# Performance work log

Measured on AMD Instinct MI355X. Metric: run time of the kernel, lower is better.

## Reference

```python
import jax, jax.numpy as jnp
from jax import lax
import numpy as np
import math

D = 256; H = 4; DH = 64; PERIOD = 30; WIN = 4; L = 2
AUDIO = 768; MOTION = 33
B = 8; T = 1024; S = 1024


def _pe_table(t, d=D, period=PERIOD):
    pos = np.arange(period, dtype=np.float32)[:, None]
    div = np.exp(np.arange(0, d, 2, dtype=np.float32) * (-math.log(10000.0) / d))
    pe = np.zeros((period, d), np.float32)
    pe[:, 0::2] = np.sin(pos * div)
    pe[:, 1::2] = np.cos(pos * div)
    reps = t // period + 1
    return jnp.asarray(np.tile(pe, (reps, 1))[:t])


def _tgt_mask(t):
    # ALiBi-style bias (quantized by period) + causal mask, per head. [H,t,t]
    slopes = jnp.array([0.25 ** (i + 1) for i in range(H)], jnp.float32)
    i = jnp.arange(t)[:, None]
    j = jnp.arange(t)[None, :]
    rel = i - j
    alibi = jnp.where(rel >= 0, -(rel // PERIOD).astype(jnp.float32), 0.0)
    causal = jnp.where(rel >= 0, 0.0, -jnp.inf)
    return slopes[:, None, None] * alibi + causal[None]


def _mem_mask(t, s):
    i = jnp.arange(t)[:, None]
    j = jnp.arange(s)[None, :]
    return jnp.where(jnp.abs(i - j) <= WIN, 0.0, -jnp.inf)


def _ln(x, g, b, eps=1e-5):
    mu = jnp.mean(x, -1, keepdims=True)
    var = jnp.mean(jnp.square(x - mu), -1, keepdims=True)
    return (x - mu) * lax.rsqrt(var + eps) * g + b


def _mha(xq, xkv, in_w, in_b, out_w, out_b, mask):
    wq, wk, wv = jnp.split(in_w, 3, axis=0)
    bq, bk, bv = jnp.split(in_b, 3)
    q = xq @ wq.T + bq
    k = xkv @ wk.T + bk
    v = xkv @ wv.T + bv
    b_, t_, _ = q.shape
    s_ = k.shape[1]
    q = q.reshape(b_, t_, H, DH)
    k = k.reshape(b_, s_, H, DH)
    v = v.reshape(b_, s_, H, DH)
    scores = jnp.einsum('bthd,bshd->bhts', q, k) / math.sqrt(DH) + mask
    a = jax.nn.softmax(scores, axis=-1)
    o = jnp.einsum('bhts,bshd->bthd', a, v).reshape(b_, t_, D)
    return o @ out_w.T + out_b


def _conv1d(x_nch, w, b):
    y = lax.conv_general_dilated(x_nch, w, (1,), [(2, 2)],
                                 dimension_numbers=('NCH', 'OIH', 'NCH'))
    return y + b[None, :, None]


def setup_inputs() -> dict:
    key = jax.random.key(0)
    ks = iter(jax.random.split(key, 40))

    def r(shape, s=0.05):
        return jax.random.normal(next(ks), shape, jnp.float32) * s

    return {
        'hidden_states': jax.random.normal(next(ks), (B, S, AUDIO), jnp.float32),
        'target_motions': jax.random.uniform(next(ks), (B, T, MOTION), jnp.float32),
        'W_af': r((D, AUDIO)), 'b_af': r((D,)),
        'conv1_w': r((D, D, 5)), 'conv1_b': r((D,)),
        'conv2_w': r((D, D, 5)), 'conv2_b': r((D,)),
        'W_vm': r((D, MOTION)), 'b_vm': r((D,)),
        'sa_in_w': r((L, 3 * D, D)), 'sa_in_b': r((L, 3 * D)),
        'sa_out_w': r((L, D, D)), 'sa_out_b': r((L, D)),
        'ca_in_w': r((L, 3 * D, D)), 'ca_in_b': r((L, 3 * D)),
        'ca_out_w': r((L, D, D)), 'ca_out_b': r((L, D)),
        'ln1_g': jnp.ones((L, D)), 'ln1_b': jnp.zeros((L, D)),
        'ln2_g': jnp.ones((L, D)), 'ln2_b': jnp.zeros((L, D)),
        'ln3_g': jnp.ones((L, D)), 'ln3_b': jnp.zeros((L, D)),
        'ff1_w': r((L, 2 * D, D)), 'ff1_b': r((L, 2 * D)),
        'ff2_w': r((L, D, 2 * D)), 'ff2_b': r((L, D)),
        'W_vr': r((MOTION, D)), 'b_vr': r((MOTION,)),
    }


def reference(hidden_states, target_motions, W_af, b_af, conv1_w, conv1_b,
              conv2_w, conv2_b, W_vm, b_vm, sa_in_w, sa_in_b, sa_out_w,
              sa_out_b, ca_in_w, ca_in_b, ca_out_w, ca_out_b, ln1_g, ln1_b,
              ln2_g, ln2_b, ln3_g, ln3_b, ff1_w, ff1_b, ff2_w, ff2_b,
              W_vr, b_vr):
    # audio encoder: linear + residual temporal convs (exact GELU)
    audio = hidden_states @ W_af.T + b_af                       # [B,S,D]
    c = _conv1d(audio.transpose(0, 2, 1), conv1_w, conv1_b)
    c = jax.nn.gelu(c, approximate=False)
    c = _conv1d(c, conv2_w, conv2_b)
    audio = audio + c.transpose(0, 2, 1)

    b_, t_, _ = target_motions.shape
    motion_in = jnp.concatenate(
        [jnp.zeros((b_, 1, MOTION), target_motions.dtype),
         target_motions[:, :-1]], axis=1)
    x = motion_in @ W_vm.T + b_vm + _pe_table(t_)               # PPE (eval: no dropout)

    tm = _tgt_mask(t_)                                          # [H,t,t]
    mm = _mem_mask(t_, audio.shape[1])                          # [t,s]

    for l in range(L):  # post-norm TransformerDecoderLayer, relu FFN
        x = _ln(x + _mha(x, x, sa_in_w[l], sa_in_b[l], sa_out_w[l], sa_out_b[l], tm),
                ln1_g[l], ln1_b[l])
        x = _ln(x + _mha(x, audio, ca_in_w[l], ca_in_b[l], ca_out_w[l], ca_out_b[l], mm),
                ln2_g[l], ln2_b[l])
        h = jax.nn.relu(x @ ff1_w[l].T + ff1_b[l]) @ ff2_w[l].T + ff2_b[l]
        x = _ln(x + h, ln3_g[l], ln3_b[l])

    return jnp.clip(x @ W_vr.T + b_vr, 0.0, 1.0)
```

## Files before the change

### kernel.cpp

```cpp
#include <hip/hip_runtime.h>
#include <math.h>

#define B_ 8
#define T_ 1024
#define S_ 1024
#define D_ 256
#define H_ 4
#define DH_ 64
#define AUDIO_ 768
#define MOTION_ 33
#define PERIOD_ 30
#define WIN_ 4
#define M_ (B_ * T_)

typedef _Float16 half8 __attribute__((ext_vector_type(8)));
typedef _Float16 half4 __attribute__((ext_vector_type(4)));
typedef __attribute__((ext_vector_type(4))) float f32x4;

#define O_AF    0
#define O_SAIN  196608
#define O_SAOUT 589824
#define O_CAIN  720896
#define O_CAOUT 1114112
#define O_FF1   1245184
#define O_FF2   1507328
#define O_CONV1 1769472
#define O_CONV2 2097152
#define O_VR    2424832
#define WH_TOT  2441216
#define HID_TOT 6291456

struct CvtSrc { const float* p[17]; };

__global__ __launch_bounds__(256) void cvt_all(
    CvtSrc s, _Float16* __restrict__ wH, _Float16* __restrict__ hidH) {
  const long i = (long)blockIdx.x * 256 + threadIdx.x;
  if (i >= (long)WH_TOT + HID_TOT) return;
  if (i >= WH_TOT) { const long j = i - WH_TOT; hidH[j] = (_Float16)s.p[15][j]; return; }
  if (i >= O_VR) {
    const long j = i - O_VR, oc = j >> 8, cin = j & 255;
    wH[i] = (oc < MOTION_) ? (_Float16)s.p[16][oc * 256 + cin] : (_Float16)0.f;
    return;
  }
  if (i >= O_CONV2) {
    const long j = i - O_CONV2, oc = j / 1280, r = j % 1280, tap = r >> 8, cin = r & 255;
    wH[i] = (_Float16)s.p[14][(oc * 256 + cin) * 5 + tap]; return;
  }
  if (i >= O_CONV1) {
    const long j = i - O_CONV1, oc = j / 1280, r = j % 1280, tap = r >> 8, cin = r & 255;
    wH[i] = (_Float16)s.p[13][(oc * 256 + cin) * 5 + tap]; return;
  }
  int seg; long base;
  if      (i >= 1638400) { seg = 12; base = 1638400; }
  else if (i >= 1507328) { seg = 11; base = 1507328; }
  else if (i >= 1376256) { seg = 10; base = 1376256; }
  else if (i >= 1245184) { seg = 9;  base = 1245184; }
  else if (i >= 1179648) { seg = 8;  base = 1179648; }
  else if (i >= 1114112) { seg = 7;  base = 1114112; }
  else if (i >= 917504)  { seg = 6;  base = 917504; }
  else if (i >= 720896)  { seg = 5;  base = 720896; }
  else if (i >= 655360)  { seg = 4;  base = 655360; }
  else if (i >= 589824)  { seg = 3;  base = 589824; }
  else if (i >= 393216)  { seg = 2;  base = 393216; }
  else if (i >= 196608)  { seg = 1;  base = 196608; }
  else                   { seg = 0;  base = 0; }
  wH[i] = (_Float16)s.p[seg][i - base];
}

__global__ __launch_bounds__(256) void gemm_h(
    const _Float16* __restrict__ A, const _Float16* __restrict__ W,
    const float* __restrict__ bias, float* __restrict__ Cf,
    _Float16* __restrict__ Ch, int M, int N, int K, int relu) {
  __shared__ _Float16 As[2][64][72];
  __shared__ _Float16 Bs[2][64][72];
  const int tid = threadIdx.x;
  const int wave = tid >> 6, lane = tid & 63;
  const int wr = wave >> 1, wc = wave & 1;
  const int lr16 = lane & 15, kq = lane >> 4;
  const int bm = blockIdx.x, bn = blockIdx.y;
  const int sr = tid >> 2, sq = tid & 3;

  const _Float16* Ap = A + (size_t)(bm * 64 + sr) * K + sq * 8;
  const _Float16* Wp = W + (size_t)(bn * 64 + sr) * K + sq * 8;

  half8 ra0 = *reinterpret_cast<const half8*>(Ap);
  half8 ra1 = *reinterpret_cast<const half8*>(Ap + 32);
  half8 rw0 = *reinterpret_cast<const half8*>(Wp);
  half8 rw1 = *reinterpret_cast<const half8*>(Wp + 32);
  f32x4 acc[2][2] = {};

  *reinterpret_cast<half8*>(&As[0][sr][sq * 8]) = ra0;
  *reinterpret_cast<half8*>(&As[0][sr][32 + sq * 8]) = ra1;
  *reinterpret_cast<half8*>(&Bs[0][sr][sq * 8]) = rw0;
  *reinterpret_cast<half8*>(&Bs[0][sr][32 + sq * 8]) = rw1;
  __syncthreads();

  const int nsteps = K >> 6;
  for (int step = 0; step < nsteps; ++step) {
    const int cur = step & 1;
    const bool more = (step + 1 < nsteps);
    if (more) {
      const int kn = (step + 1) << 6;
      ra0 = *reinterpret_cast<const half8*>(Ap + kn);
      ra1 = *reinterpret_cast<const half8*>(Ap + kn + 32);
      rw0 = *reinterpret_cast<const half8*>(Wp + kn);
      rw1 = *reinterpret_cast<const half8*>(Wp + kn + 32);
    }
    half8 af[2][2], bf[2][2];
#pragma unroll
    for (int m = 0; m < 2; ++m)
#pragma unroll
      for (int s = 0; s < 2; ++s)
        af[m][s] = *reinterpret_cast<const half8*>(
            &As[cur][wr * 32 + m * 16 + lr16][s * 32 + kq * 8]);
#pragma unroll
    for (int n = 0; n < 2; ++n)
#pragma unroll
      for (int s = 0; s < 2; ++s)
        bf[n][s] = *reinterpret_cast<const half8*>(
            &Bs[cur][wc * 32 + n * 16 + lr16][s * 32 + kq * 8]);
#pragma unroll
    for (int m = 0; m < 2; ++m)
#pragma unroll
      for (int n = 0; n < 2; ++n)
#pragma unroll
        for (int s = 0; s < 2; ++s)
          acc[m][n] = __builtin_amdgcn_mfma_f32_16x16x32_f16(af[m][s], bf[n][s], acc[m][n], 0, 0, 0);
    if (more) {
      *reinterpret_cast<half8*>(&As[cur ^ 1][sr][sq * 8]) = ra0;
      *reinterpret_cast<half8*>(&As[cur ^ 1][sr][32 + sq * 8]) = ra1;
      *reinterpret_cast<half8*>(&Bs[cur ^ 1][sr][sq * 8]) = rw0;
      *reinterpret_cast<half8*>(&Bs[cur ^ 1][sr][32 + sq * 8]) = rw1;
      __syncthreads();
    }
  }

#pragma unroll
  for (int m = 0; m < 2; ++m) {
#pragma unroll
    for (int n = 0; n < 2; ++n) {
      const int col = bn * 64 + wc * 32 + n * 16 + lr16;
      const float bv = bias[col];
#pragma unroll
      for (int j = 0; j < 4; ++j) {
        const int row = bm * 64 + wr * 32 + m * 16 + kq * 4 + j;
        float v = acc[m][n][j] + bv;
        if (relu) v = fmaxf(v, 0.f);
        const size_t idx = (size_t)row * N + col;
        if (Cf) Cf[idx] = v;
        if (Ch) Ch[idx] = (_Float16)v;
      }
    }
  }
}

__global__ __launch_bounds__(256) void gemm_ca(
    const _Float16* __restrict__ Aq, const _Float16* __restrict__ Akv,
    const _Float16* __restrict__ W, const float* __restrict__ bias,
    _Float16* __restrict__ Oq, _Float16* __restrict__ Okv) {
  __shared__ _Float16 As[2][64][72];
  __shared__ _Float16 Bs[2][64][72];
  const int tid = threadIdx.x;
  const int wave = tid >> 6, lane = tid & 63;
  const int wr = wave >> 1, wc = wave & 1;
  const int lr16 = lane & 15, kq = lane >> 4;
  const int bm = blockIdx.x, bn = blockIdx.y;
  const int sr = tid >> 2, sq = tid & 3;
  const bool isq = (bn < 4);
  const _Float16* A = isq ? Aq : Akv;
  _Float16* Optr = isq ? Oq : Okv;
  const int Nout = isq ? 256 : 512;
  const int ocol0 = (isq ? bn : bn - 4) * 64;

  const _Float16* Ap = A + (size_t)(bm * 64 + sr) * 256 + sq * 8;
  const _Float16* Wp = W + (size_t)(bn * 64 + sr) * 256 + sq * 8;

  half8 ra0 = *reinterpret_cast<const half8*>(Ap);
  half8 ra1 = *reinterpret_cast<const half8*>(Ap + 32);
  half8 rw0 = *reinterpret_cast<const half8*>(Wp);
  half8 rw1 = *reinterpret_cast<const half8*>(Wp + 32);
  f32x4 acc[2][2] = {};

  *reinterpret_cast<half8*>(&As[0][sr][sq * 8]) = ra0;
  *reinterpret_cast<half8*>(&As[0][sr][32 + sq * 8]) = ra1;
  *reinterpret_cast<half8*>(&Bs[0][sr][sq * 8]) = rw0;
  *reinterpret_cast<half8*>(&Bs[0][sr][32 + sq * 8]) = rw1;
  __syncthreads();

  for (int step = 0; step < 4; ++step) {
    const int cur = step & 1;
    const bool more = (step + 1 < 4);
    if (more) {
      const int kn = (step + 1) << 6;
      ra0 = *reinterpret_cast<const half8*>(Ap + kn);
      ra1 = *reinterpret_cast<const half8*>(Ap + kn + 32);
      rw0 = *reinterpret_cast<const half8*>(Wp + kn);
      rw1 = *reinterpret_cast<const half8*>(Wp + kn + 32);
    }
    half8 af[2][2], bf[2][2];
#pragma unroll
    for (int m = 0; m < 2; ++m)
#pragma unroll
      for (int s = 0; s < 2; ++s)
        af[m][s] = *reinterpret_cast<const half8*>(
            &As[cur][wr * 32 + m * 16 + lr16][s * 32 + kq * 8]);
#pragma unroll
    for (int n = 0; n < 2; ++n)
#pragma unroll
      for (int s = 0; s < 2; ++s)
        bf[n][s] = *reinterpret_cast<const half8*>(
            &Bs[cur][wc * 32 + n * 16 + lr16][s * 32 + kq * 8]);
#pragma unroll
    for (int m = 0; m < 2; ++m)
#pragma unroll
      for (int n = 0; n < 2; ++n)
#pragma unroll
        for (int s = 0; s < 2; ++s)
          acc[m][n] = __builtin_amdgcn_mfma_f32_16x16x32_f16(af[m][s], bf[n][s], acc[m][n], 0, 0, 0);
    if (more) {
      *reinterpret_cast<half8*>(&As[cur ^ 1][sr][sq * 8]) = ra0;
      *reinterpret_cast<half8*>(&As[cur ^ 1][sr][32 + sq * 8]) = ra1;
      *reinterpret_cast<half8*>(&Bs[cur ^ 1][sr][sq * 8]) = rw0;
      *reinterpret_cast<half8*>(&Bs[cur ^ 1][sr][32 + sq * 8]) = rw1;
      __syncthreads();
    }
  }

#pragma unroll
  for (int m = 0; m < 2; ++m) {
#pragma unroll
    for (int n = 0; n < 2; ++n) {
      const int lc = wc * 32 + n * 16 + lr16;
      const float bv = bias[bn * 64 + lc];
#pragma unroll
      for (int j = 0; j < 4; ++j) {
        const int row = bm * 64 + wr * 32 + m * 16 + kq * 4 + j;
        Optr[(size_t)row * Nout + ocol0 + lc] = (_Float16)(acc[m][n][j] + bv);
      }
    }
  }
}

__device__ __forceinline__ half8 conv_ld(const _Float16* Xb, int p, int tap, int cin) {
  const int sp = p + tap - 2;
  if (sp < 0 || sp >= S_) { half8 z = {}; return z; }
  return *reinterpret_cast<const half8*>(Xb + (size_t)sp * D_ + cin);
}

__global__ __launch_bounds__(256) void conv_h(
    const _Float16* __restrict__ Xh, const _Float16* __restrict__ Wc,
    const float* __restrict__ bias, _Float16* OutH,
    const _Float16* ResH, int mode) {
  __shared__ _Float16 As[2][64][72];
  __shared__ _Float16 Bs[2][64][72];
  const int tid = threadIdx.x;
  const int wave = tid >> 6, lane = tid & 63;
  const int wr = wave >> 1, wc = wave & 1;
  const int lr16 = lane & 15, kq = lane >> 4;
  const int b = blockIdx.x >> 4;
  const int s0 = (blockIdx.x & 15) * 64;
  const int o0 = blockIdx.y * 64;
  const int sr = tid >> 2, sq = tid & 3;

  const _Float16* Xb = Xh + (size_t)b * S_ * D_;
  const _Float16* Wp = Wc + (size_t)(o0 + sr) * 1280 + sq * 8;
  const int p = s0 + sr;

  half8 ra0 = conv_ld(Xb, p, 0, sq * 8);
  half8 ra1 = conv_ld(Xb, p, 0, 32 + sq * 8);
  half8 rw0 = *reinterpret_cast<const half8*>(Wp);
  half8 rw1 = *reinterpret_cast<const half8*>(Wp + 32);
  f32x4 acc[2][2] = {};

  *reinterpret_cast<half8*>(&As[0][sr][sq * 8]) = ra0;
  *reinterpret_cast<half8*>(&As[0][sr][32 + sq * 8]) = ra1;
  *reinterpret_cast<half8*>(&Bs[0][sr][sq * 8]) = rw0;
  *reinterpret_cast<half8*>(&Bs[0][sr][32 + sq * 8]) = rw1;
  __syncthreads();

  for (int step = 0; step < 20; ++step) {
    const int cur = step & 1;
    const bool more = (step + 1 < 20);
    if (more) {
      const int kn = (step + 1) << 6;
      const int tap = kn >> 8, cb = kn & 255;
      ra0 = conv_ld(Xb, p, tap, cb + sq * 8);
      ra1 = conv_ld(Xb, p, tap, cb + 32 + sq * 8);
      rw0 = *reinterpret_cast<const half8*>(Wp + kn);
      rw1 = *reinterpret_cast<const half8*>(Wp + kn + 32);
    }
    half8 af[2][2], bf[2][2];
#pragma unroll
    for (int m = 0; m < 2; ++m)
#pragma unroll
      for (int s = 0; s < 2; ++s)
        af[m][s] = *reinterpret_cast<const half8*>(
            &As[cur][wr * 32 + m * 16 + lr16][s * 32 + kq * 8]);
#pragma unroll
    for (int n = 0; n < 2; ++n)
#pragma unroll
      for (int s = 0; s < 2; ++s)
        bf[n][s] = *reinterpret_cast<const half8*>(
            &Bs[cur][wc * 32 + n * 16 + lr16][s * 32 + kq * 8]);
#pragma unroll
    for (int m = 0; m < 2; ++m)
#pragma unroll
      for (int n = 0; n < 2; ++n)
#pragma unroll
        for (int s = 0; s < 2; ++s)
          acc[m][n] = __builtin_amdgcn_mfma_f32_16x16x32_f16(af[m][s], bf[n][s], acc[m][n], 0, 0, 0);
    if (more) {
      *reinterpret_cast<half8*>(&As[cur ^ 1][sr][sq * 8]) = ra0;
      *reinterpret_cast<half8*>(&As[cur ^ 1][sr][32 + sq * 8]) = ra1;
      *reinterpret_cast<half8*>(&Bs[cur ^ 1][sr][sq * 8]) = rw0;
      *reinterpret_cast<half8*>(&Bs[cur ^ 1][sr][32 + sq * 8]) = rw1;
      __syncthreads();
    }
  }

#pragma unroll
  for (int m = 0; m < 2; ++m) {
#pragma unroll
    for (int n = 0; n < 2; ++n) {
      const int oc = o0 + wc * 32 + n * 16 + lr16;
      const float bv = bias[oc];
#pragma unroll
      for (int j = 0; j < 4; ++j) {
        const int s = s0 + wr * 32 + m * 16 + kq * 4 + j;
        const size_t idx = ((size_t)b * S_ + s) * D_ + oc;
        float v = acc[m][n][j] + bv;
        if (mode == 0) {
          v = 0.5f * v * (1.f + erff(v * 0.70710678118654752f));
        } else {
          v += (float)ResH[idx];
        }
        OutH[idx] = (_Float16)v;
      }
    }
  }
}

__global__ __launch_bounds__(256) void head_mfma(
    const _Float16* __restrict__ Xh, const _Float16* __restrict__ Wh,
    const float* __restrict__ bv, float* __restrict__ Out) {
  __shared__ _Float16 As[2][64][72];
  __shared__ _Float16 Bs[2][64][72];
  const int tid = threadIdx.x;
  const int wave = tid >> 6, lane = tid & 63;
  const int wr = wave >> 1, wc = wave & 1;
  const int lr16 = lane & 15, kq = lane >> 4;
  const int bm = blockIdx.x;
  const int sr = tid >> 2, sq = tid & 3;

  const _Float16* Ap = Xh + (size_t)(bm * 64 + sr) * D_ + sq * 8;
  const _Float16* Wp = Wh + (size_t)sr * D_ + sq * 8;

  half8 ra0 = *reinterpret_cast<const half8*>(Ap);
  half8 ra1 = *reinterpret_cast<const half8*>(Ap + 32);
  half8 rw0 = *reinterpret_cast<const half8*>(Wp);
  half8 rw1 = *reinterpret_cast<const half8*>(Wp + 32);
  f32x4 acc[2][2] = {};

  *reinterpret_cast<half8*>(&As[0][sr][sq * 8]) = ra0;
  *reinterpret_cast<half8*>(&As[0][sr][32 + sq * 8]) = ra1;
  *reinterpret_cast<half8*>(&Bs[0][sr][sq * 8]) = rw0;
  *reinterpret_cast<half8*>(&Bs[0][sr][32 + sq * 8]) = rw1;
  __syncthreads();

  for (int step = 0; step < 4; ++step) {
    const int cur = step & 1;
    const bool more = (step + 1 < 4);
    if (more) {
      const int kn = (step + 1) << 6;
      ra0 = *reinterpret_cast<const half8*>(Ap + kn);
      ra1 = *reinterpret_cast<const half8*>(Ap + kn + 32);
      rw0 = *reinterpret_cast<const half8*>(Wp + kn);
      rw1 = *reinterpret_cast<const half8*>(Wp + kn + 32);
    }
    half8 af[2][2], bf[2][2];
#pragma unroll
    for (int m = 0; m < 2; ++m)
#pragma unroll
      for (int s = 0; s < 2; ++s)
        af[m][s] = *reinterpret_cast<const half8*>(
            &As[cur][wr * 32 + m * 16 + lr16][s * 32 + kq * 8]);
#pragma unroll
    for (int n = 0; n < 2; ++n)
#pragma unroll
      for (int s = 0; s < 2; ++s)
        bf[n][s] = *reinterpret_cast<const half8*>(
            &Bs[cur][wc * 32 + n * 16 + lr16][s * 32 + kq * 8]);
#pragma unroll
    for (int m = 0; m < 2; ++m)
#pragma unroll
      for (int n = 0; n < 2; ++n)
#pragma unroll
        for (int s = 0; s < 2; ++s)
          acc[m][n] = __builtin_amdgcn_mfma_f32_16x16x32_f16(af[m][s], bf[n][s], acc[m][n], 0, 0, 0);
    if (more) {
      *reinterpret_cast<half8*>(&As[cur ^ 1][sr][sq * 8]) = ra0;
      *reinterpret_cast<half8*>(&As[cur ^ 1][sr][32 + sq * 8]) = ra1;
      *reinterpret_cast<half8*>(&Bs[cur ^ 1][sr][sq * 8]) = rw0;
      *reinterpret_cast<half8*>(&Bs[cur ^ 1][sr][32 + sq * 8]) = rw1;
      __syncthreads();
    }
  }

#pragma unroll
  for (int m = 0; m < 2; ++m) {
#pragma unroll
    for (int n = 0; n < 2; ++n) {
      const int col = wc * 32 + n * 16 + lr16;
      if (col < MOTION_) {
        const float bb = bv[col];
#pragma unroll
        for (int j = 0; j < 4; ++j) {
          const int row = bm * 64 + wr * 32 + m * 16 + kq * 4 + j;
          float v = acc[m][n][j] + bb;
          Out[(size_t)row * MOTION_ + col] = fminf(fmaxf(v, 0.f), 1.f);
        }
      }
    }
  }
}

__global__ __launch_bounds__(256) void motion_pe(
    const float* __restrict__ TM, const float* __restrict__ Wvm,
    const float* __restrict__ bvm, float* __restrict__ Xout,
    _Float16* __restrict__ XoutH) {
  const int d = threadIdx.x;
  const int bt = blockIdx.x;
  const int t = bt & (T_ - 1);
  const int b = bt >> 10;
  float acc = bvm[d];
  if (t > 0) {
    const float* mrow = TM + ((size_t)b * T_ + t - 1) * MOTION_;
    const float* wrow = Wvm + (size_t)d * MOTION_;
#pragma unroll
    for (int m = 0; m < MOTION_; ++m) acc += mrow[m] * wrow[m];
  }
  const int pos = t % PERIOD_;
  const int i2 = d >> 1;
  const float div = expf((float)(2 * i2) * (-9.210340371976184f / 256.f));
  const float ang = (float)pos * div;
  acc += (d & 1) ? cosf(ang) : sinf(ang);
  Xout[(size_t)bt * D_ + d] = acc;
  XoutH[(size_t)bt * D_ + d] = (_Float16)acc;
}

#define RSK_ 72
#define RSV_ 64
__global__ __launch_bounds__(512) void self_attn(
    const _Float16* __restrict__ QKV, _Float16* __restrict__ O) {
  __shared__ _Float16 Ks[2][64 * RSK_];
  __shared__ _Float16 VTs[2][64 * RSV_];
  __shared__ _Float16 Ps[8][16 * RSK_];
  const int qtb = blockIdx.x, h = blockIdx.y, b = blockIdx.z;
  const int tid = threadIdx.x;
  const int wave = tid >> 6, lane = tid & 63;
  const int lo = lane & 15, hi = lane >> 4;
  const float slope = exp2f(-2.f * (float)(h + 1));
  const int qloc = wave * 16 + lo;
  const int tq = qtb * 128 + qloc;
  const size_t base = (size_t)b * T_ * 768 + h * 64;
  const int sj = tid >> 3, sch = tid & 7;

  half8 qf[2];
#pragma unroll
  for (int s = 0; s < 2; ++s)
    qf[s] = *reinterpret_cast<const half8*>(
        QKV + base + (size_t)(qtb * 128 + qloc) * 768 + s * 32 + hi * 8);

  f32x4 oacc[4] = {};
  float mrun = -1e30f, lrun = 0.f;

  const int nkt = 2 * qtb + 2;

  half8 rk, rv;
  {
    const size_t rowoff = base + (size_t)sj * 768;
    rk = *reinterpret_cast<const half8*>(QKV + rowoff + 256 + sch * 8);
    rv = *reinterpret_cast<const half8*>(QKV + rowoff + 512 + sch * 8);
    *reinterpret_cast<half8*>(&Ks[0][sj * RSK_ + sch * 8]) = rk;
#pragma unroll
    for (int r = 0; r < 8; ++r) {
      const int d = sch * 8 + r;
      const int sw = ((d & 7) ^ (d >> 3)) << 3;
      VTs[0][d * RSV_ + (sj ^ sw)] = rv[r];
    }
  }
  __syncthreads();

  for (int kt = 0; kt < nkt; ++kt) {
    const int cur = kt & 1;
    const bool more = (kt + 1 < nkt);
    if (more) {
      const size_t rowoff = base + (size_t)((kt + 1) * 64 + sj) * 768;
      rk = *reinterpret_cast<const half8*>(QKV + rowoff + 256 + sch * 8);
      rv = *reinterpret_cast<const half8*>(QKV + rowoff + 512 + sch * 8);
    }

    f32x4 st[4] = {};
#pragma unroll
    for (int f = 0; f < 4; ++f) {
#pragma unroll
      for (int s = 0; s < 2; ++s) {
        const half8 kf = *reinterpret_cast<const half8*>(
            &Ks[cur][(f * 16 + lo) * RSK_ + s * 32 + hi * 8]);
        st[f] = __builtin_amdgcn_mfma_f32_16x16x32_f16(kf, qf[s], st[f], 0, 0, 0);
      }
    }

    float sc[4][4];
    float tmax = -1e30f;
#pragma unroll
    for (int f = 0; f < 4; ++f)
#pragma unroll
      for (int r = 0; r < 4; ++r) {
        const int j = kt * 64 + f * 16 + hi * 4 + r;
        const int rel = tq - j;
        const float v = (rel >= 0)
            ? st[f][r] * 0.125f - slope * (float)(rel / PERIOD_) : -1e30f;
        sc[f][r] = v;
        tmax = fmaxf(tmax, v);
      }
    tmax = fmaxf(tmax, __shfl_xor(tmax, 16, 64));
    tmax = fmaxf(tmax, __shfl_xor(tmax, 32, 64));
    const float mnew = fmaxf(mrun, tmax);
    const float scale = __expf(mrun - mnew);

    float psum = 0.f;
#pragma unroll
    for (int f = 0; f < 4; ++f) {
      half4 ph;
#pragma unroll
      for (int r = 0; r < 4; ++r) {
        const float pv = __expf(sc[f][r] - mnew);
        psum += pv;
        ph[r] = (_Float16)pv;
      }
      *reinterpret_cast<half4*>(&Ps[wave][lo * RSK_ + f * 16 + hi * 4]) = ph;
    }
    psum += __shfl_xor(psum, 16, 64);
    psum += __shfl_xor(psum, 32, 64);
    lrun = lrun * scale + psum;
    mrun = mnew;

    float rsc[4];
#pragma unroll
    for (int r = 0; r < 4; ++r) rsc[r] = __shfl(scale, hi * 4 + r, 64);
#pragma unroll
    for (int nf = 0; nf < 4; ++nf)
#pragma unroll
      for (int r = 0; r < 4; ++r) oacc[nf][r] *= rsc[r];

#pragma unroll
    for (int s = 0; s < 2; ++s) {
      const half8 pf = *reinterpret_cast<const half8*>(
          &Ps[wave][lo * RSK_ + s * 32 + hi * 8]);
#pragma unroll
      for (int nf = 0; nf < 4; ++nf) {
        const int d = nf * 16 + lo;
        const int sw = ((d & 7) ^ (d >> 3)) << 3;
        const half8 vf = *reinterpret_cast<const half8*>(
            &VTs[cur][d * RSV_ + ((s * 32 + hi * 8) ^ sw)]);
        oacc[nf] = __builtin_amdgcn_mfma_f32_16x16x32_f16(pf, vf, oacc[nf], 0, 0, 0);
      }
    }

    if (more) {
      *reinterpret_cast<half8*>(&Ks[cur ^ 1][sj * RSK_ + sch * 8]) = rk;
#pragma unroll
      for (int r = 0; r < 8; ++r) {
        const int d = sch * 8 + r;
        const int sw = ((d & 7) ^ (d >> 3)) << 3;
        VTs[cur ^ 1][d * RSV_ + (sj ^ sw)] = rv[r];
      }
      __syncthreads();
    }
  }

  float invl[4];
#pragma unroll
  for (int r = 0; r < 4; ++r) invl[r] = 1.f / __shfl(lrun, hi * 4 + r, 64);
#pragma unroll
  for (int nf = 0; nf < 4; ++nf)
#pragma unroll
    for (int r = 0; r < 4; ++r) {
      const int q = qtb * 128 + wave * 16 + hi * 4 + r;
      O[((size_t)b * T_ + q) * D_ + h * 64 + nf * 16 + lo] =
          (_Float16)(oacc[nf][r] * invl[r]);
    }
}

__global__ __launch_bounds__(128) void cross_attn(
    const _Float16* __restrict__ Q, const _Float16* __restrict__ KV,
    _Float16* __restrict__ O) {
  const int gid = blockIdx.x * 128 + threadIdx.x;
  const int h = gid & 3;
  const int bt = gid >> 2;
  const int t = bt & (T_ - 1);
  const int b = bt >> 10;

  float q[64];
  const _Float16* qp = Q + (size_t)bt * D_ + h * 64;
#pragma unroll
  for (int d0 = 0; d0 < 64; d0 += 8) {
    const half8 v = *reinterpret_cast<const half8*>(qp + d0);
#pragma unroll
    for (int e = 0; e < 8; ++e) q[d0 + e] = (float)v[e];
  }

  const int j0 = (t - WIN_ > 0) ? t - WIN_ : 0;
  const int j1 = (t + WIN_ < S_ - 1) ? t + WIN_ : S_ - 1;
  const int nj = j1 - j0 + 1;

  float sc[9];
  float mx = -1e30f;
#pragma unroll
  for (int jj = 0; jj < 9; ++jj) {
    if (jj < nj) {
      const _Float16* kp = KV + ((size_t)b * S_ + j0 + jj) * 512 + h * 64;
      float s = 0.f;
#pragma unroll
      for (int d0 = 0; d0 < 64; d0 += 8) {
        const half8 kv = *reinterpret_cast<const half8*>(kp + d0);
#pragma unroll
        for (int e = 0; e < 8; ++e) s += q[d0 + e] * (float)kv[e];
      }
      sc[jj] = s * 0.125f;
      mx = fmaxf(mx, sc[jj]);
    } else {
      sc[jj] = -1e30f;
    }
  }
  float l = 0.f;
  float p[9];
#pragma unroll
  for (int jj = 0; jj < 9; ++jj) { p[jj] = __expf(sc[jj] - mx); l += p[jj]; }
  const float inv = 1.f / l;

  float o[64];
#pragma unroll
  for (int d = 0; d < 64; ++d) o[d] = 0.f;
#pragma unroll
  for (int jj = 0; jj < 9; ++jj) {
    if (jj < nj) {
      const float pj = p[jj] * inv;
      const _Float16* vp = KV + ((size_t)b * S_ + j0 + jj) * 512 + 256 + h * 64;
#pragma unroll
      for (int d0 = 0; d0 < 64; d0 += 8) {
        const half8 vv = *reinterpret_cast<const half8*>(vp + d0);
#pragma unroll
        for (int e = 0; e < 8; ++e) o[d0 + e] += pj * (float)vv[e];
      }
    }
  }
  _Float16* op = O + (size_t)bt * D_ + h * 64;
#pragma unroll
  for (int d = 0; d < 64; ++d) op[d] = (_Float16)o[d];
}

__global__ __launch_bounds__(256) void ln_res(
    const float* X, const _Float16* __restrict__ R,
    const float* __restrict__ g, const float* __restrict__ bta,
    float* Out, _Float16* __restrict__ OutH) {
  const int wid = threadIdx.x >> 6, lane = threadIdx.x & 63;
  const size_t row = (size_t)blockIdx.x * 4 + wid;
  const float* xp = X + row * D_;
  const _Float16* rp = R + row * D_;
  float v[4];
  float s = 0.f;
#pragma unroll
  for (int k = 0; k < 4; ++k) {
    const int d = lane + k * 64;
    v[k] = xp[d] + (float)rp[d];
    s += v[k];
  }
#pragma unroll
  for (int off = 32; off; off >>= 1) s += __shfl_xor(s, off, 64);
  const float mu = s * (1.f / 256.f);
  float var = 0.f;
#pragma unroll
  for (int k = 0; k < 4; ++k) { const float d = v[k] - mu; var += d * d; }
#pragma unroll
  for (int off = 32; off; off >>= 1) var += __shfl_xor(var, off, 64);
  const float rs = rsqrtf(var * (1.f / 256.f) + 1e-5f);
#pragma unroll
  for (int k = 0; k < 4; ++k) {
    const int d = lane + k * 64;
    const float o = (v[k] - mu) * rs * g[d] + bta[d];
    Out[row * D_ + d] = o;
    OutH[row * D_ + d] = (_Float16)o;
  }
}

extern "C" void kernel_launch(void* const* d_in, const int* in_sizes, int n_in,
                              void* d_out, int out_size, void* d_ws, size_t ws_size,
                              hipStream_t stream) {
  (void)in_sizes; (void)n_in; (void)out_size; (void)ws_size;
  const float* hidden = (const float*)d_in[0];
  const float* tmot   = (const float*)d_in[1];
  const float* W_af   = (const float*)d_in[2];
  const float* b_af   = (const float*)d_in[3];
  const float* c1w    = (const float*)d_in[4];
  const float* c1b    = (const float*)d_in[5];
  const float* c2w    = (const float*)d_in[6];
  const float* c2b    = (const float*)d_in[7];
  const float* Wvm    = (const float*)d_in[8];
  const float* bvm    = (const float*)d_in[9];
  const float* sa_in_w  = (const float*)d_in[10];
  const float* sa_in_b  = (const float*)d_in[11];
  const float* sa_out_w = (const float*)d_in[12];
  const float* sa_out_b = (const float*)d_in[13];
  const float* ca_in_w  = (const float*)d_in[14];
  const float* ca_in_b  = (const float*)d_in[15];
  const float* ca_out_w = (const float*)d_in[16];
  const float* ca_out_b = (const float*)d_in[17];
  const float* ln1g = (const float*)d_in[18];
  const float* ln1b = (const float*)d_in[19];
  const float* ln2g = (const float*)d_in[20];
  const float* ln2b = (const float*)d_in[21];
  const float* ln3g = (const float*)d_in[22];
  const float* ln3b = (const float*)d_in[23];
  const float* ff1w = (const float*)d_in[24];
  const float* ff1b = (const float*)d_in[25];
  const float* ff2w = (const float*)d_in[26];
  const float* ff2b = (const float*)d_in[27];
  const float* Wvr  = (const float*)d_in[28];
  const float* bvr  = (const float*)d_in[29];
  float* out = (float*)d_out;

  float* ws = (float*)d_ws;
  const size_t BSD = (size_t)M_ * D_;
  float* x     = ws + BSD;
  _Float16* t1h = (_Float16*)(ws + 2 * BSD);
  _Float16* hb = (_Float16*)(ws + 3 * BSD);
  _Float16* Rh      = hb;
  _Float16* x_h     = hb + 3 * BSD;
  _Float16* audio_h = hb + 4 * BSD;
  _Float16* att_h   = hb + 5 * BSD;
  _Float16* wH      = hb + 6 * BSD;
  _Float16* ckv_h   = Rh + BSD;

  const dim3 blk(256);

  CvtSrc cs;
  cs.p[0] = W_af;
  cs.p[1] = sa_in_w;            cs.p[2] = sa_in_w + 768 * 256;
  cs.p[3] = sa_out_w;           cs.p[4] = sa_out_w + 256 * 256;
  cs.p[5] = ca_in_w;            cs.p[6] = ca_in_w + 768 * 256;
  cs.p[7] = ca_out_w;           cs.p[8] = ca_out_w + 256 * 256;
  cs.p[9] = ff1w;               cs.p[10] = ff1w + 512 * 256;
  cs.p[11] = ff2w;              cs.p[12] = ff2w + 256 * 512;
  cs.p[13] = c1w;               cs.p[14] = c2w;
  cs.p[15] = hidden;            cs.p[16] = Wvr;
  cvt_all<<<dim3((WH_TOT + HID_TOT + 255) / 256), blk, 0, stream>>>(cs, wH, Rh);

  gemm_h<<<dim3(M_ / 64, 4), blk, 0, stream>>>(Rh, wH + O_AF, b_af, nullptr, audio_h,
                                               M_, 256, 768, 0);
  conv_h<<<dim3(128, 4), blk, 0, stream>>>(audio_h, wH + O_CONV1, c1b, t1h, nullptr, 0);
  conv_h<<<dim3(128, 4), blk, 0, stream>>>(t1h, wH + O_CONV2, c2b, audio_h, audio_h, 1);

  motion_pe<<<dim3(M_), blk, 0, stream>>>(tmot, Wvm, bvm, x, x_h);

  for (int l = 0; l < 2; ++l) {
    gemm_h<<<dim3(M_ / 64, 12), blk, 0, stream>>>(
        x_h, wH + O_SAIN + l * 196608, sa_in_b + l * 768, nullptr, Rh, M_, 768, 256, 0);
    self_attn<<<dim3(T_ / 128, H_, B_), dim3(512), 0, stream>>>(Rh, att_h);
    gemm_h<<<dim3(M_ / 64, 4), blk, 0, stream>>>(
        att_h, wH + O_SAOUT + l * 65536, sa_out_b + l * 256, nullptr, t1h, M_, 256, 256, 0);
    ln_res<<<dim3(M_ / 4), blk, 0, stream>>>(x, t1h, ln1g + l * 256, ln1b + l * 256, x, x_h);

    gemm_ca<<<dim3(M_ / 64, 12), blk, 0, stream>>>(
        x_h, audio_h, wH + O_CAIN + l * 196608, ca_in_b + l * 768, Rh, ckv_h);
    cross_attn<<<dim3(M_ * H_ / 128), dim3(128), 0, stream>>>(Rh, ckv_h, att_h);
    gemm_h<<<dim3(M_ / 64, 4), blk, 0, stream>>>(
        att_h, wH + O_CAOUT + l * 65536, ca_out_b + l * 256, nullptr, t1h, M_, 256, 256, 0);
    ln_res<<<dim3(M_ / 4), blk, 0, stream>>>(x, t1h, ln2g + l * 256, ln2b + l * 256, x, x_h);

    gemm_h<<<dim3(M_ / 64, 8), blk, 0, stream>>>(
        x_h, wH + O_FF1 + l * 131072, ff1b + l * 512, nullptr, Rh, M_, 512, 256, 1);
    gemm_h<<<dim3(M_ / 64, 4), blk, 0, stream>>>(
        Rh, wH + O_FF2 + l * 131072, ff2b + l * 256, nullptr, t1h, M_, 256, 512, 0);
    ln_res<<<dim3(M_ / 4), blk, 0, stream>>>(x, t1h, ln3g + l * 256, ln3b + l * 256, x, x_h);
  }

  head_mfma<<<dim3(M_ / 64), blk, 0, stream>>>(x_h, wH + O_VR, bvr, out);
}
```

Baseline: 334.9 us.

## Fuse output-projection GEMMs with residual add and LayerNorm into one kernel

```diff
diff --git a/kernel.cpp b/kernel.cpp
--- a/kernel.cpp
+++ b/kernel.cpp
@@ -151,6 +151,110 @@
         if (Ch) Ch[idx] = (_Float16)v;
       }
     }
+  }
+}
+
+__global__ __launch_bounds__(256) void gemm_ln(
+    const _Float16* __restrict__ A, const _Float16* __restrict__ W,
+    const float* __restrict__ bias, const float* __restrict__ g,
+    const float* __restrict__ bta, float* x, _Float16* __restrict__ x_h,
+    int K) {
+  __shared__ __align__(16) char smem[4608 + 36864];
+  _Float16 (*As)[72] = reinterpret_cast<_Float16(*)[72]>(smem);
+  _Float16 (*Bs)[72] = reinterpret_cast<_Float16(*)[72]>(smem + 4608);
+  float (*Vt)[260]   = reinterpret_cast<float(*)[260]>(smem + 4608);
+  const int tid = threadIdx.x;
+  const int wave = tid >> 6, lane = tid & 63;
+  const int lo = lane & 15, hi = lane >> 4;
+  const int wc64 = wave * 64;
+  const int bm = blockIdx.x;
+  const int sr = tid >> 3, sq = tid & 7;
+
+  const _Float16* Ap = A + (size_t)(bm * 32 + sr) * K + sq * 8;
+  const _Float16* Wp = W + sq * 8;
+
+  f32x4 acc[2][4] = {};
+  half8 ra;
+  half8 rb[8];
+
+  const int nsteps = K >> 6;
+  ra = *reinterpret_cast<const half8*>(Ap);
+#pragma unroll
+  for (int i = 0; i < 8; ++i)
+    rb[i] = *reinterpret_cast<const half8*>(Wp + (size_t)(sr + i * 32) * K);
+
+  for (int step = 0; step < nsteps; ++step) {
+    if (step > 0) __syncthreads();
+    *reinterpret_cast<half8*>(&As[sr][sq * 8]) = ra;
+#pragma unroll
+    for (int i = 0; i < 8; ++i)
+      *reinterpret_cast<half8*>(&Bs[sr + i * 32][sq * 8]) = rb[i];
+    __syncthreads();
+    if (step + 1 < nsteps) {
+      const int kn = (step + 1) << 6;
+      ra = *reinterpret_cast<const half8*>(Ap + kn);
+#pragma unroll
+      for (int i = 0; i < 8; ++i)
+        rb[i] = *reinterpret_cast<const half8*>(Wp + (size_t)(sr + i * 32) * K + kn);
+    }
+    half8 af[2][2], bf[4][2];
+#pragma unroll
+    for (int rf = 0; rf < 2; ++rf)
+#pragma unroll
+      for (int s = 0; s < 2; ++s)
+        af[rf][s] = *reinterpret_cast<const half8*>(
+            &As[rf * 16 + lo][s * 32 + hi * 8]);
+#pragma unroll
+    for (int n = 0; n < 4; ++n)
+#pragma unroll
+      for (int s = 0; s < 2; ++s)
+        bf[n][s] = *reinterpret_cast<const half8*>(
+            &Bs[wc64 + n * 16 + lo][s * 32 + hi * 8]);
+#pragma unroll
+    for (int rf = 0; rf < 2; ++rf)
+#pragma unroll
+      for (int n = 0; n < 4; ++n)
+#pragma unroll
+        for (int s = 0; s < 2; ++s)
+          acc[rf][n] = __builtin_amdgcn_mfma_f32_16x16x32_f16(af[rf][s], bf[n][s], acc[rf][n], 0, 0, 0);
+  }
+
+  __syncthreads();
+
+#pragma unroll
+  for (int rf = 0; rf < 2; ++rf) {
+#pragma unroll
+    for (int n = 0; n < 4; ++n) {
+      const int col = wc64 + n * 16 + lo;
+      const float bv = bias[col];
+#pragma unroll
+      for (int j = 0; j < 4; ++j) {
+        const int row = rf * 16 + hi * 4 + j;
+        Vt[row][col] = acc[rf][n][j] + bv + x[(size_t)(bm * 32 + row) * D_ + col];
+      }
+    }
+  }
+  __syncthreads();
+
+  const int row = tid >> 3, sub = tid & 7;
+  float s = 0.f, s2 = 0.f;
+#pragma unroll
+  for (int i = 0; i < 32; ++i) {
+    const float v = Vt[row][sub * 32 + i];
+    s += v; s2 += v * v;
+  }
+  s += __shfl_xor(s, 1, 64);  s += __shfl_xor(s, 2, 64);  s += __shfl_xor(s, 4, 64);
+  s2 += __shfl_xor(s2, 1, 64); s2 += __shfl_xor(s2, 2, 64); s2 += __shfl_xor(s2, 4, 64);
+  const float mu = s * (1.f / 256.f);
+  const float var = s2 * (1.f / 256.f) - mu * mu;
+  const float rs = rsqrtf(var + 1e-5f);
+  const size_t grow = (size_t)(bm * 32 + row) * D_;
+#pragma unroll
+  for (int i = 0; i < 32; ++i) {
+    const int c = sub * 32 + i;
+    const float o = (Vt[row][c] - mu) * rs * g[c] + bta[c];
+    x[grow + c] = o;
+    x_h[grow + c] = (_Float16)o;
   }
 }
 
@@ -659,40 +763,6 @@
   _Float16* op = O + (size_t)bt * D_ + h * 64;
 #pragma unroll
   for (int d = 0; d < 64; ++d) op[d] = (_Float16)o[d];
-}
-
-__global__ __launch_bounds__(256) void ln_res(
-    const float* X, const _Float16* __restrict__ R,
-    const float* __restrict__ g, const float* __restrict__ bta,
-    float* Out, _Float16* __restrict__ OutH) {
-  const int wid = threadIdx.x >> 6, lane = threadIdx.x & 63;
-  const size_t row = (size_t)blockIdx.x * 4 + wid;
-  const float* xp = X + row * D_;
-  const _Float16* rp = R + row * D_;
-  float v[4];
-  float s = 0.f;
-#pragma unroll
-  for (int k = 0; k < 4; ++k) {
-    const int d = lane + k * 64;
-    v[k] = xp[d] + (float)rp[d];
-    s += v[k];
-  }
-#pragma unroll
-  for (int off = 32; off; off >>= 1) s += __shfl_xor(s, off, 64);
-  const float mu = s * (1.f / 256.f);
-  float var = 0.f;
-#pragma unroll
-  for (int k = 0; k < 4; ++k) { const float d = v[k] - mu; var += d * d; }
-#pragma unroll
-  for (int off = 32; off; off >>= 1) var += __shfl_xor(var, off, 64);
-  const float rs = rsqrtf(var * (1.f / 256.f) + 1e-5f);
-#pragma unroll
-  for (int k = 0; k < 4; ++k) {
-    const int d = lane + k * 64;
-    const float o = (v[k] - mu) * rs * g[d] + bta[d];
-    Out[row * D_ + d] = o;
-    OutH[row * D_ + d] = (_Float16)o;
-  }
 }
 
 extern "C" void kernel_launch(void* const* d_in, const int* in_sizes, int n_in,
@@ -768,22 +838,22 @@
     gemm_h<<<dim3(M_ / 64, 12), blk, 0, stream>>>(
         x_h, wH + O_SAIN + l * 196608, sa_in_b + l * 768, nullptr, Rh, M_, 768, 256, 0);
     self_attn<<<dim3(T_ / 128, H_, B_), dim3(512), 0, stream>>>(Rh, att_h);
-    gemm_h<<<dim3(M_ / 64, 4), blk, 0, stream>>>(
-        att_h, wH + O_SAOUT + l * 65536, sa_out_b + l * 256, nullptr, t1h, M_, 256, 256, 0);
-    ln_res<<<dim3(M_ / 4), blk, 0, stream>>>(x, t1h, ln1g + l * 256, ln1b + l * 256, x, x_h);
+    gemm_ln<<<dim3(M_ / 32), blk, 0, stream>>>(
+        att_h, wH + O_SAOUT + l * 65536, sa_out_b + l * 256,
+        ln1g + l * 256, ln1b + l * 256, x, x_h, 256);
 
     gemm_ca<<<dim3(M_ / 64, 12), blk, 0, stream>>>(
         x_h, audio_h, wH + O_CAIN + l * 196608, ca_in_b + l * 768, Rh, ckv_h);
     cross_attn<<<dim3(M_ * H_ / 128), dim3(128), 0, stream>>>(Rh, ckv_h, att_h);
-    gemm_h<<<dim3(M_ / 64, 4), blk, 0, stream>>>(
-        att_h, wH + O_CAOUT + l * 65536, ca_out_b + l * 256, nullptr, t1h, M_, 256, 256, 0);
-    ln_res<<<dim3(M_ / 4), blk, 0, stream>>>(x, t1h, ln2g + l * 256, ln2b + l * 256, x, x_h);
+    gemm_ln<<<dim3(M_ / 32), blk, 0, stream>>>(
+        att_h, wH + O_CAOUT + l * 65536, ca_out_b + l * 256,
+        ln2g + l * 256, ln2b + l * 256, x, x_h, 256);
 
     gemm_h<<<dim3(M_ / 64, 8), blk, 0, stream>>>(
         x_h, wH + O_FF1 + l * 131072, ff1b + l * 512, nullptr, Rh, M_, 512, 256, 1);
-    gemm_h<<<dim3(M_ / 64, 4), blk, 0, stream>>>(
-        Rh, wH + O_FF2 + l * 131072, ff2b + l * 256, nullptr, t1h, M_, 256, 512, 0);
-    ln_res<<<dim3(M_ / 4), blk, 0, stream>>>(x, t1h, ln3g + l * 256, ln3b + l * 256, x, x_h);
+    gemm_ln<<<dim3(M_ / 32), blk, 0, stream>>>(
+        Rh, wH + O_FF2 + l * 131072, ff2b + l * 256,
+        ln3g + l * 256, ln3b + l * 256, x, x_h, 512);
   }
 
   head_mfma<<<dim3(M_ / 64), blk, 0, stream>>>(x_h, wH + O_VR, bvr, out);
```

After: 347.7 us. +3.8%, slower.
